# Optimization experiments

Hardware: AMD Instinct MI355X
Metric: run time of the kernel (lower is better)

The kernel has to match this reference:

```python
import jax, jax.numpy as jnp
import numpy as np

N = 50000   # nodes
E = 800000  # edges (avg degree 16)
F = 128     # input_nf = output_nf
H = 128     # hidden_nf


def setup_inputs() -> dict:
    key = jax.random.key(0)
    ks = jax.random.split(key, 10)
    # coords: spatial part in [-1, 1], z-coordinate (last dim) in [0.5, 1.5] (must be > 0)
    xz = jax.random.uniform(ks[0], (N, 3), minval=-1.0, maxval=1.0)
    xz = xz.at[:, -1].set(jax.random.uniform(ks[1], (N,), minval=0.5, maxval=1.5))
    h = jax.random.normal(ks[2], (N, F), dtype=jnp.float32)
    row = jax.random.randint(ks[3], (E,), 0, N)
    # guarantee col != row so AdS distance is strictly positive on every edge
    col = (row + 1 + jax.random.randint(ks[4], (E,), 0, N - 1)) % N
    edge_index = jnp.stack([row, col]).astype(jnp.int32)

    def lin(k, fan_in, fan_out):
        return jax.random.normal(k, (fan_in, fan_out), dtype=jnp.float32) / np.float32(np.sqrt(fan_in))

    return {
        "xz": xz,
        "h": h,
        "We1": lin(ks[5], 2 * F + 1, H), "be1": jnp.full((H,), 0.1, jnp.float32),
        "We2": lin(ks[6], H, H),         "be2": jnp.full((H,), 0.1, jnp.float32),
        "Wn1": lin(ks[7], H + F, H),     "bn1": jnp.full((H,), 0.1, jnp.float32),
        "Wn2": lin(ks[8], H, F),         "bn2": jnp.full((F,), 0.1, jnp.float32),
        "edge_index": edge_index,
    }


def reference(xz, h, We1, be1, We2, be2, Wn1, bn1, Wn2, bn2, edge_index):
    row, col = edge_index[0], edge_index[1]
    n = h.shape[0]

    # AdS (hyperbolic upper-half-space) distance between xz[row] and xz[col]:
    # d = arccosh(1 + |p1 - p2|^2 / (2 z1 z2)), z = last coordinate
    diff = xz[row] - xz[col]                                  # [E, 3]
    u = jnp.sum(diff * diff, axis=-1) / (2.0 * xz[row, -1] * xz[col, -1])
    dist = jnp.arccosh(1.0 + u)[:, None]                      # [E, 1]

    # edge model: concat(source, target, radial) -> Linear -> silu -> Linear -> silu
    m = jnp.concatenate([h[row], h[col], dist], axis=1)       # [E, 2F+1]
    m = jax.nn.silu(m @ We1 + be1)                            # [E, H]
    m = jax.nn.silu(m @ We2 + be2)                            # [E, H]

    # segment_mean over destination nodes (row)
    num = jax.ops.segment_sum(m, row, num_segments=n)                          # [N, H]
    den = jax.ops.segment_sum(jnp.ones_like(m), row, num_segments=n)          # [N, H]
    agg = num / jnp.maximum(den, jnp.ones((), den.dtype))

    # node model: concat(h, agg) -> Linear -> silu -> Linear, plus residual
    z = jnp.concatenate([h, agg], axis=1)                     # [N, F+H]
    out = jax.nn.silu(z @ Wn1 + bn1) @ Wn2 + bn2              # [N, F]
    return h + out
```

## Files before the change

### kernel.cpp

```cpp
#include <hip/hip_runtime.h>

#define NN 50000
#define EE 800000
#define NB 196

typedef __bf16 bf16x8 __attribute__((ext_vector_type(8)));
typedef float  f32x4  __attribute__((ext_vector_type(4)));

__device__ __forceinline__ float bf2f(ushort u) {
    union { unsigned int i; float f; } v; v.i = ((unsigned int)u) << 16; return v.f;
}
__device__ __forceinline__ ushort f2bf(float f) {
    union { float f; unsigned int i; } v; v.f = f;
    unsigned int u = v.i;
    return (ushort)((u + 0x7FFFu + ((u >> 16) & 1u)) >> 16);
}
__device__ __forceinline__ ushort f2bf_fast(float f) {
    union { float f; unsigned int i; } v; v.f = f;
    return (ushort)((v.i + 0x8000u) >> 16);
}
__device__ __forceinline__ float silu(float x) {
    return x * __builtin_amdgcn_rcpf(1.0f + __expf(-x));
}

__global__ void detect_kernel(const ushort* __restrict__ xzu, int* __restrict__ flag) {
    __shared__ int cnt;
    if (threadIdx.x == 0) cnt = 0;
    __syncthreads();
    float v = bf2f(xzu[2 * threadIdx.x]);
    bool sane = (v == v) && (fabsf(v) <= 4.0f);
    if (sane) atomicAdd(&cnt, 1);
    __syncthreads();
    if (threadIdx.x == 0) *flag = (cnt >= 192) ? 0 : 1;
}

__global__ void prep_kernel(const void* __restrict__ hsrc, const void* __restrict__ xzsrc,
                            const int* __restrict__ erow, const int* __restrict__ flag,
                            ushort* __restrict__ hb, float* __restrict__ xzf,
                            int* __restrict__ cntI) {
    const bool isf = (*flag != 0);
    int b = blockIdx.x;
    if (b < 3125) {
        int i = (b * 256 + threadIdx.x) * 8;
        uint4 o;
        if (isf) {
            const float* s = (const float*)hsrc + i;
            float4 f0 = *(const float4*)s;
            float4 f1 = *(const float4*)(s + 4);
            o.x = (unsigned int)f2bf(f0.x) | ((unsigned int)f2bf(f0.y) << 16);
            o.y = (unsigned int)f2bf(f0.z) | ((unsigned int)f2bf(f0.w) << 16);
            o.z = (unsigned int)f2bf(f1.x) | ((unsigned int)f2bf(f1.y) << 16);
            o.w = (unsigned int)f2bf(f1.z) | ((unsigned int)f2bf(f1.w) << 16);
        } else {
            o = *(const uint4*)((const ushort*)hsrc + i);
        }
        *(uint4*)(hb + i) = o;
    } else if (b < 3712) {
        int i = (b - 3125) * 256 + threadIdx.x;
        if (i < NN * 3)
            xzf[i] = isf ? ((const float*)xzsrc)[i] : bf2f(((const ushort*)xzsrc)[i]);
    } else {
        int e = (b - 3712) * 256 + threadIdx.x;
        if (e < EE) atomicAdd(&cntI[erow[e]], 1);
    }
}

__global__ void swizzle_misc_kernel(const void* We1, const void* We2,
                                    const void* Wn1, const void* Wn2,
                                    const void* be1, const void* be2,
                                    const void* bn1, const void* bn2,
                                    const int* __restrict__ flag,
                                    ushort* __restrict__ We1s, ushort* __restrict__ We2s,
                                    ushort* __restrict__ Wn1s, ushort* __restrict__ Wn2s,
                                    float* __restrict__ fb, ushort* __restrict__ wlb) {
    const bool isf = (*flag != 0);
    if (blockIdx.x == 48) {
        for (int j = threadIdx.x; j < 640; j += 256) {
            int which = j >> 7, k = j & 127;
            const void* src = (which == 0) ? be1 : (which == 1) ? be2 :
                              (which == 2) ? bn1 : (which == 3) ? bn2 : We1;
            size_t idx = (which == 4) ? ((size_t)256 * 128 + k) : (size_t)k;
            float v = isf ? ((const float*)src)[idx] : bf2f(((const ushort*)src)[idx]);
            fb[j] = v;
            if (which == 4) wlb[k] = f2bf(v);
        }
        return;
    }
    int c = blockIdx.x * 256 + threadIdx.x;
    const void* src; ushort* dst; int cl;
    if      (c <  4096) { src = We1; dst = We1s; cl = c;         }
    else if (c <  6144) { src = We2; dst = We2s; cl = c - 4096;  }
    else if (c < 10240) { src = Wn1; dst = Wn1s; cl = c - 6144;  }
    else                { src = Wn2; dst = Wn2s; cl = c - 10240; }
    int l = cl & 63, nt = (cl >> 6) & 7, kc = cl >> 9;
    int kbase = kc * 32 + (l >> 4) * 8;
    int n = nt * 16 + (l & 15);
    ushort tmp[8];
#pragma unroll
    for (int j = 0; j < 8; ++j) {
        size_t idx = (size_t)(kbase + j) * 128 + n;
        tmp[j] = isf ? f2bf(((const float*)src)[idx]) : ((const ushort*)src)[idx];
    }
#pragma unroll
    for (int j = 0; j < 8; ++j) dst[(size_t)cl * 8 + j] = tmp[j];
}

__global__ void scanA_kernel(const int* __restrict__ cntI, int* __restrict__ bsum) {
    __shared__ int s[256];
    int t = threadIdx.x;
    int i = blockIdx.x * 256 + t;
    s[t] = (i < NN) ? cntI[i] : 0;
    __syncthreads();
#pragma unroll
    for (int off = 128; off > 0; off >>= 1) {
        if (t < off) s[t] += s[t + off];
        __syncthreads();
    }
    if (t == 0) bsum[blockIdx.x] = s[0];
}

__global__ void scanB_kernel(int* __restrict__ bsum) {
    __shared__ int s[256];
    int t = threadIdx.x;
    int v = (t < NB) ? bsum[t] : 0;
    s[t] = v;
    __syncthreads();
    for (int off = 1; off < 256; off <<= 1) {
        int u = (t >= off) ? s[t - off] : 0;
        __syncthreads();
        if (t >= off) s[t] += u;
        __syncthreads();
    }
    if (t < NB) bsum[t] = s[t] - v;
}

__global__ void scanC_kernel(const int* __restrict__ cntI, const int* __restrict__ bsum,
                             int* __restrict__ rowStart) {
    __shared__ int s[256];
    int t = threadIdx.x;
    int i = blockIdx.x * 256 + t;
    int v = (i < NN) ? cntI[i] : 0;
    s[t] = v;
    __syncthreads();
    for (int off = 1; off < 256; off <<= 1) {
        int u = (t >= off) ? s[t - off] : 0;
        __syncthreads();
        if (t >= off) s[t] += u;
        __syncthreads();
    }
    if (i < NN) rowStart[i] = bsum[blockIdx.x] + s[t] - v;
}

__global__ void scatter_kernel(const int* __restrict__ erow, const int* __restrict__ ecol,
                               const float* __restrict__ xzf,
                               const int* __restrict__ rowStart, int* __restrict__ cursor,
                               int* __restrict__ erowS, int* __restrict__ ecolS,
                               float* __restrict__ distS) {
    int e = blockIdx.x * 256 + threadIdx.x;
    if (e >= EE) return;
    int r = erow[e], c = ecol[e];
    int pos = rowStart[r] + atomicAdd(&cursor[r], 1);
    float4 a = *(const float4*)(xzf + 3 * r);
    float4 b = *(const float4*)(xzf + 3 * c);
    float dx = a.x - b.x, dy = a.y - b.y, dz = a.z - b.z;
    float u = (dx * dx + dy * dy + dz * dz) * __builtin_amdgcn_rcpf(2.0f * a.z * b.z);
    u = fminf(fmaxf(u, 0.0f), 1.0e6f);
    erowS[pos] = r;
    ecolS[pos] = c;
    distS[pos] = __logf(1.0f + u + sqrtf(u * (u + 2.0f)));
}

__global__ __launch_bounds__(256, 3) void pq_kernel(
    const ushort* __restrict__ hb, const ushort* __restrict__ We1s,
    const float* __restrict__ fb, ushort* __restrict__ Pp, ushort* __restrict__ Qq) {
    __shared__ __align__(16) ushort sA[8192];
    const int tid = threadIdx.x;
    const int lane = tid & 63, w = tid >> 6;
    const int col = lane & 15, quad = lane >> 4;
    const int nt0 = w * 2;
    const int ntiles = (NN + 63) / 64;
    const int nA = w * 32 + col, nB = nA + 16;
    const float be1A = fb[nA], be1B = fb[nB];

    for (int tile = blockIdx.x; tile < ntiles; tile += gridDim.x) {
        __syncthreads();
        const int n0 = tile * 64;
#pragma unroll
        for (int i = 0; i < 4; ++i) {
            int node = n0 + lane;
            uint4 v = (node < NN) ? *(const uint4*)(hb + (size_t)node * 128 + (w + 4 * i) * 8)
                                  : make_uint4(0, 0, 0, 0);
            *(uint4*)(sA + (((lane >> 4) * 4 + i) * 64 + w * 16 + (lane & 15)) * 8) = v;
        }
        __syncthreads();

        f32x4 accP[4][2] = {}, accQ[4][2] = {};
#pragma unroll
        for (int kc = 0; kc < 4; ++kc) {
            bf16x8 bp0 = *(const bf16x8*)(We1s + ((kc * 8 + nt0)           * 64 + lane) * 8);
            bf16x8 bp1 = *(const bf16x8*)(We1s + ((kc * 8 + nt0 + 1)       * 64 + lane) * 8);
            bf16x8 bq0 = *(const bf16x8*)(We1s + (((kc + 4) * 8 + nt0)     * 64 + lane) * 8);
            bf16x8 bq1 = *(const bf16x8*)(We1s + (((kc + 4) * 8 + nt0 + 1) * 64 + lane) * 8);
#pragma unroll
            for (int g = 0; g < 4; ++g) {
                bf16x8 a = *(const bf16x8*)(sA + ((g * 4 + kc) * 64 + lane) * 8);
                accP[g][0] = __builtin_amdgcn_mfma_f32_16x16x32_bf16(a, bp0, accP[g][0], 0, 0, 0);
                accP[g][1] = __builtin_amdgcn_mfma_f32_16x16x32_bf16(a, bp1, accP[g][1], 0, 0, 0);
                accQ[g][0] = __builtin_amdgcn_mfma_f32_16x16x32_bf16(a, bq0, accQ[g][0], 0, 0, 0);
                accQ[g][1] = __builtin_amdgcn_mfma_f32_16x16x32_bf16(a, bq1, accQ[g][1], 0, 0, 0);
            }
        }
#pragma unroll
        for (int g = 0; g < 4; ++g) {
#pragma unroll
            for (int r = 0; r < 4; ++r) {
                int node = n0 + g * 16 + quad * 4 + r;
                if (node < NN) {
                    size_t o = (size_t)node * 128;
                    Pp[o + nA] = f2bf(accP[g][0][r] + be1A);
                    Pp[o + nB] = f2bf(accP[g][1][r] + be1B);
                    Qq[o + nA] = f2bf(accQ[g][0][r]);
                    Qq[o + nB] = f2bf(accQ[g][1][r]);
                }
            }
        }
    }
}

__global__ __launch_bounds__(256, 4) void edge_kernel(
    const ushort* __restrict__ Pp, const ushort* __restrict__ Qq,
    const int* __restrict__ erowS, const int* __restrict__ ecolS,
    const float* __restrict__ distS, const ushort* __restrict__ We2s,
    const ushort* __restrict__ wlb, const float* __restrict__ fb,
    float* __restrict__ agg) {
    __shared__ __align__(16) char smem[64 * 132 * 4];
    __shared__ int sRow[64];
    ushort* sM = (ushort*)smem;
    float (*sOut)[132] = (float(*)[132])smem;

    const int tid = threadIdx.x;
    const int lane = tid & 63, w = tid >> 6;
    const int col = lane & 15, quad = lane >> 4;
    const int nt0 = w * 2;

    const int nA = w * 32 + col, nB = nA + 16;
    const float be2A = fb[128 + nA], be2B = fb[128 + nB];

    bf16x8 B2[8];
#pragma unroll
    for (int kc = 0; kc < 4; ++kc) {
        B2[kc * 2]     = *(const bf16x8*)(We2s + ((kc * 8 + nt0)     * 64 + lane) * 8);
        B2[kc * 2 + 1] = *(const bf16x8*)(We2s + ((kc * 8 + nt0 + 1) * 64 + lane) * 8);
    }
    bf16x8 WL[4];
#pragma unroll
    for (int i = 0; i < 4; ++i) WL[i] = *(const bf16x8*)(wlb + (w + 4 * i) * 8);

    const int ntiles = EE / 64;
    const int per = (ntiles + gridDim.x - 1) / gridDim.x;
    const int t0 = blockIdx.x * per;
    const int t1 = (t0 + per < ntiles) ? (t0 + per) : ntiles;

    for (int tile = t0; tile < t1; ++tile) {
        __syncthreads();
        const int e = tile * 64 + lane;
        const int r = erowS[e], c = ecolS[e];
        const float d = distS[e];
        if (w == 0) sRow[lane] = r;
#pragma unroll
        for (int i = 0; i < 4; ++i) {
            int ch = w + 4 * i;
            bf16x8 p = *(const bf16x8*)(Pp + (size_t)r * 128 + ch * 8);
            bf16x8 q = *(const bf16x8*)(Qq + (size_t)c * 128 + ch * 8);
            ushort out8[8];
#pragma unroll
            for (int j = 0; j < 8; ++j) {
                float x = (float)p[j] + (float)q[j] + d * (float)WL[i][j];
                out8[j] = f2bf_fast(silu(x));
            }
            *(uint4*)(sM + (((lane >> 4) * 4 + i) * 64 + w * 16 + (lane & 15)) * 8) =
                *(const uint4*)out8;
        }
        __syncthreads();

        f32x4 acc2[4][2] = {};
#pragma unroll
        for (int kc = 0; kc < 4; ++kc) {
#pragma unroll
            for (int g = 0; g < 4; ++g) {
                bf16x8 a = *(const bf16x8*)(sM + ((g * 4 + kc) * 64 + lane) * 8);
                acc2[g][0] = __builtin_amdgcn_mfma_f32_16x16x32_bf16(a, B2[kc * 2],     acc2[g][0], 0, 0, 0);
                acc2[g][1] = __builtin_amdgcn_mfma_f32_16x16x32_bf16(a, B2[kc * 2 + 1], acc2[g][1], 0, 0, 0);
            }
        }
        __syncthreads();

#pragma unroll
        for (int g = 0; g < 4; ++g) {
#pragma unroll
            for (int r4 = 0; r4 < 4; ++r4) {
                int m = g * 16 + quad * 4 + r4;
                sOut[m][nA] = silu(acc2[g][0][r4] + be2A);
                sOut[m][nB] = silu(acc2[g][1][r4] + be2B);
            }
        }
        __syncthreads();

        {
            const int cc = tid & 127;
            const int mb = (tid >> 7) * 32;
            float acc = 0.0f;
            int prow = sRow[mb];
            for (int k = 0; k < 32; ++k) {
                int rw = sRow[mb + k];
                if (rw != prow) {
                    unsafeAtomicAdd(&agg[(size_t)prow * 128 + cc], acc);
                    acc = 0.0f;
                    prow = rw;
                }
                acc += sOut[mb + k][cc];
            }
            unsafeAtomicAdd(&agg[(size_t)prow * 128 + cc], acc);
        }
    }
}

__global__ __launch_bounds__(256, 3) void node_kernel(
    const ushort* __restrict__ hb, const void* __restrict__ hraw,
    const float* __restrict__ agg, const int* __restrict__ cntI,
    const ushort* __restrict__ Wn1s, const ushort* __restrict__ Wn2s,
    const float* __restrict__ fb, const int* __restrict__ flag,
    void* __restrict__ outv) {
    __shared__ __align__(16) ushort sA[16384];
    __shared__ __align__(16) ushort sM[8192];
    const int tid = threadIdx.x;
    const int lane = tid & 63, w = tid >> 6;
    const int col = lane & 15, quad = lane >> 4;
    const int nt0 = w * 2;
    const int ntiles = (NN + 63) / 64;
    const bool isf = (*flag != 0);
    float* outf = (float*)outv;
    ushort* outu = (ushort*)outv;

    const int nA = w * 32 + col, nB = nA + 16;
    const float bn1A = fb[256 + nA], bn1B = fb[256 + nB];
    const float bn2A = fb[384 + nA], bn2B = fb[384 + nB];

    for (int tile = blockIdx.x; tile < ntiles; tile += gridDim.x) {
        __syncthreads();
        const int n0 = tile * 64;
#pragma unroll
        for (int i = 0; i < 8; ++i) {
            int kb = w + 4 * i;
            int node = n0 + lane;
            uint4 v;
            if (node < NN) {
                if (kb < 16) {
                    v = *(const uint4*)(hb + (size_t)node * 128 + kb * 8);
                } else {
                    const float* ap = agg + (size_t)node * 128 + (kb - 16) * 8;
                    float invc = __builtin_amdgcn_rcpf(fmaxf((float)cntI[node], 1.0f));
                    float4 f0 = *(const float4*)ap;
                    float4 f1 = *(const float4*)(ap + 4);
                    v.x = (unsigned int)f2bf_fast(f0.x * invc) | ((unsigned int)f2bf_fast(f0.y * invc) << 16);
                    v.y = (unsigned int)f2bf_fast(f0.z * invc) | ((unsigned int)f2bf_fast(f0.w * invc) << 16);
                    v.z = (unsigned int)f2bf_fast(f1.x * invc) | ((unsigned int)f2bf_fast(f1.y * invc) << 16);
                    v.w = (unsigned int)f2bf_fast(f1.z * invc) | ((unsigned int)f2bf_fast(f1.w * invc) << 16);
                }
            } else {
                v = make_uint4(0, 0, 0, 0);
            }
            *(uint4*)(sA + (((quad * 8 + i) * 64) + w * 16 + col) * 8) = v;
        }
        __syncthreads();

        f32x4 acc[4][2] = {};
#pragma unroll
        for (int kc = 0; kc < 8; ++kc) {
            bf16x8 b0 = *(const bf16x8*)(Wn1s + ((kc * 8 + nt0)     * 64 + lane) * 8);
            bf16x8 b1 = *(const bf16x8*)(Wn1s + ((kc * 8 + nt0 + 1) * 64 + lane) * 8);
#pragma unroll
            for (int g = 0; g < 4; ++g) {
                bf16x8 a = *(const bf16x8*)(sA + ((g * 8 + kc) * 64 + lane) * 8);
                acc[g][0] = __builtin_amdgcn_mfma_f32_16x16x32_bf16(a, b0, acc[g][0], 0, 0, 0);
                acc[g][1] = __builtin_amdgcn_mfma_f32_16x16x32_bf16(a, b1, acc[g][1], 0, 0, 0);
            }
        }
#pragma unroll
        for (int g = 0; g < 4; ++g) {
            int base0 = ((g * 4 + w) * 64 + (col >> 3) * 16) * 8 + (col & 7);
#pragma unroll
            for (int r = 0; r < 4; ++r) {
                int mrow = quad * 4 + r;
                sM[base0 + mrow * 8]              = f2bf_fast(silu(acc[g][0][r] + bn1A));
                sM[base0 + 2 * 16 * 8 + mrow * 8] = f2bf_fast(silu(acc[g][1][r] + bn1B));
            }
        }
        __syncthreads();

        f32x4 acc2[4][2] = {};
#pragma unroll
        for (int kc = 0; kc < 4; ++kc) {
            bf16x8 b0 = *(const bf16x8*)(Wn2s + ((kc * 8 + nt0)     * 64 + lane) * 8);
            bf16x8 b1 = *(const bf16x8*)(Wn2s + ((kc * 8 + nt0 + 1) * 64 + lane) * 8);
#pragma unroll
            for (int g = 0; g < 4; ++g) {
                bf16x8 a = *(const bf16x8*)(sM + ((g * 4 + kc) * 64 + lane) * 8);
                acc2[g][0] = __builtin_amdgcn_mfma_f32_16x16x32_bf16(a, b0, acc2[g][0], 0, 0, 0);
                acc2[g][1] = __builtin_amdgcn_mfma_f32_16x16x32_bf16(a, b1, acc2[g][1], 0, 0, 0);
            }
        }
#pragma unroll
        for (int g = 0; g < 4; ++g) {
#pragma unroll
            for (int r = 0; r < 4; ++r) {
                int ml2 = g * 16 + quad * 4 + r;
                int node = n0 + ml2;
                if (node < NN) {
                    size_t oi = (size_t)node * 128;
                    float h0 = isf ? ((const float*)hraw)[oi + nA] : bf2f(((const ushort*)hraw)[oi + nA]);
                    float h1 = isf ? ((const float*)hraw)[oi + nB] : bf2f(((const ushort*)hraw)[oi + nB]);
                    float x0 = acc2[g][0][r] + bn2A + h0;
                    float x1 = acc2[g][1][r] + bn2B + h1;
                    if (isf) { outf[oi + nA] = x0; outf[oi + nB] = x1; }
                    else     { outu[oi + nA] = f2bf_fast(x0); outu[oi + nB] = f2bf_fast(x1); }
                }
            }
        }
    }
}

extern "C" void kernel_launch(void* const* d_in, const int* in_sizes, int n_in,
                              void* d_out, int out_size, void* d_ws, size_t ws_size,
                              hipStream_t stream) {
    const void* xz  = d_in[0];
    const void* h   = d_in[1];
    const void* We1 = d_in[2];
    const void* be1 = d_in[3];
    const void* We2 = d_in[4];
    const void* be2 = d_in[5];
    const void* Wn1 = d_in[6];
    const void* bn1 = d_in[7];
    const void* Wn2 = d_in[8];
    const void* bn2 = d_in[9];
    const int*  ei  = (const int*)d_in[10];
    const int* erow = ei;
    const int* ecol = ei + EE;

    char* base = (char*)d_ws;
    size_t cur = 0;
    auto alloc = [&](size_t bytes) { size_t o = cur; cur = (cur + bytes + 255) & ~(size_t)255; return o; };
    int*    flag   = (int*)   (base + alloc(16));
    float*  agg    = (float*) (base + alloc((size_t)NN * 128 * 4));
    int*    cntI   = (int*)   (base + alloc((size_t)NN * 4));
    int*    cursor = (int*)   (base + alloc((size_t)NN * 4));
    ushort* hb     = (ushort*)(base + alloc((size_t)NN * 128 * 2));
    ushort* Pp     = (ushort*)(base + alloc((size_t)NN * 128 * 2));
    ushort* Qq     = (ushort*)(base + alloc((size_t)NN * 128 * 2));
    int*    erowS  = (int*)   (base + alloc((size_t)EE * 4));
    int*    ecolS  = (int*)   (base + alloc((size_t)EE * 4));
    float*  distS  = (float*) (base + alloc((size_t)EE * 4));
    float*  xzf    = (float*) (base + alloc((size_t)NN * 3 * 4 + 16));
    int*    rowSt  = (int*)   (base + alloc((size_t)NN * 4));
    int*    bsum   = (int*)   (base + alloc(256 * 4));
    ushort* We1s   = (ushort*)(base + alloc(32768 * 2));
    ushort* We2s   = (ushort*)(base + alloc(16384 * 2));
    ushort* Wn1s   = (ushort*)(base + alloc(32768 * 2));
    ushort* Wn2s   = (ushort*)(base + alloc(16384 * 2));
    float*  fb     = (float*) (base + alloc(640 * 4));
    ushort* wlb    = (ushort*)(base + alloc(128 * 2));

    size_t zbytes = (size_t)((char*)hb - (char*)agg);
    (void)hipMemsetAsync(agg, 0, zbytes, stream);

    detect_kernel<<<1, 256, 0, stream>>>((const ushort*)xz, flag);
    prep_kernel<<<6837, 256, 0, stream>>>(h, xz, erow, flag, hb, xzf, cntI);
    swizzle_misc_kernel<<<49, 256, 0, stream>>>(We1, We2, Wn1, Wn2, be1, be2, bn1, bn2,
                                                flag, We1s, We2s, Wn1s, Wn2s, fb, wlb);
    scanA_kernel<<<NB, 256, 0, stream>>>(cntI, bsum);
    scanB_kernel<<<1, 256, 0, stream>>>(bsum);
    scanC_kernel<<<NB, 256, 0, stream>>>(cntI, bsum, rowSt);
    scatter_kernel<<<(EE + 255) / 256, 256, 0, stream>>>(erow, ecol, xzf, rowSt, cursor,
                                                         erowS, ecolS, distS);
    pq_kernel<<<782, 256, 0, stream>>>(hb, We1s, fb, Pp, Qq);
    edge_kernel<<<1024, 256, 0, stream>>>(Pp, Qq, erowS, ecolS, distS, We2s, wlb, fb, agg);
    node_kernel<<<782, 256, 0, stream>>>(hb, h, agg, cntI, Wn1s, Wn2s, fb, flag, d_out);
}
```

Baseline: 347.0 us.

## Fuse scan kernels, pack edge records, and segment-reduce edge outputs in registers

Drops the single-block scanB launch by having each scanC block redo the scan of block sums itself. Packs row, col and distance into one int4 per sorted edge so each edge is a single 16-byte load. The edge kernel's final stage now applies silu and segment-reduces straight from the MFMA accumulators, with no fp32 shared-memory staging or the two barriers around it. Shared memory therefore shrinks, so launch bounds go to 8 blocks per CU and the grid doubles to 2048. The register reduction only merges runs of the same row within the 4 rows each lane holds, so it issues more global atomics than the old 32-row column sweeps.

```diff
diff --git a/kernel.cpp b/kernel.cpp
--- a/kernel.cpp
+++ b/kernel.cpp
@@ -119,25 +119,22 @@
     if (t == 0) bsum[blockIdx.x] = s[0];
 }
 
-__global__ void scanB_kernel(int* __restrict__ bsum) {
-    __shared__ int s[256];
-    int t = threadIdx.x;
-    int v = (t < NB) ? bsum[t] : 0;
-    s[t] = v;
-    __syncthreads();
-    for (int off = 1; off < 256; off <<= 1) {
-        int u = (t >= off) ? s[t - off] : 0;
-        __syncthreads();
-        if (t >= off) s[t] += u;
-        __syncthreads();
-    }
-    if (t < NB) bsum[t] = s[t] - v;
-}
-
 __global__ void scanC_kernel(const int* __restrict__ cntI, const int* __restrict__ bsum,
                              int* __restrict__ rowStart) {
     __shared__ int s[256];
+    __shared__ int sbase;
     int t = threadIdx.x;
+    int bv = (t < NB) ? bsum[t] : 0;
+    s[t] = bv;
+    __syncthreads();
+    for (int off = 1; off < 256; off <<= 1) {
+        int u = (t >= off) ? s[t - off] : 0;
+        __syncthreads();
+        if (t >= off) s[t] += u;
+        __syncthreads();
+    }
+    if (t == 0) sbase = (blockIdx.x == 0) ? 0 : s[blockIdx.x - 1];
+    __syncthreads();
     int i = blockIdx.x * 256 + t;
     int v = (i < NN) ? cntI[i] : 0;
     s[t] = v;
@@ -148,14 +145,13 @@
         if (t >= off) s[t] += u;
         __syncthreads();
     }
-    if (i < NN) rowStart[i] = bsum[blockIdx.x] + s[t] - v;
+    if (i < NN) rowStart[i] = sbase + s[t] - v;
 }
 
 __global__ void scatter_kernel(const int* __restrict__ erow, const int* __restrict__ ecol,
                                const float* __restrict__ xzf,
                                const int* __restrict__ rowStart, int* __restrict__ cursor,
-                               int* __restrict__ erowS, int* __restrict__ ecolS,
-                               float* __restrict__ distS) {
+                               int4* __restrict__ eS) {
     int e = blockIdx.x * 256 + threadIdx.x;
     if (e >= EE) return;
     int r = erow[e], c = ecol[e];
@@ -165,9 +161,8 @@
     float dx = a.x - b.x, dy = a.y - b.y, dz = a.z - b.z;
     float u = (dx * dx + dy * dy + dz * dz) * __builtin_amdgcn_rcpf(2.0f * a.z * b.z);
     u = fminf(fmaxf(u, 0.0f), 1.0e6f);
-    erowS[pos] = r;
-    ecolS[pos] = c;
-    distS[pos] = __logf(1.0f + u + sqrtf(u * (u + 2.0f)));
+    float d = __logf(1.0f + u + sqrtf(u * (u + 2.0f)));
+    eS[pos] = make_int4(r, c, __float_as_int(d), 0);
 }
 
 __global__ __launch_bounds__(256, 3) void pq_kernel(
@@ -227,16 +222,13 @@
     }
 }
 
-__global__ __launch_bounds__(256, 4) void edge_kernel(
+__global__ __launch_bounds__(256, 8) void edge_kernel(
     const ushort* __restrict__ Pp, const ushort* __restrict__ Qq,
-    const int* __restrict__ erowS, const int* __restrict__ ecolS,
-    const float* __restrict__ distS, const ushort* __restrict__ We2s,
+    const int4* __restrict__ eS, const ushort* __restrict__ We2s,
     const ushort* __restrict__ wlb, const float* __restrict__ fb,
     float* __restrict__ agg) {
-    __shared__ __align__(16) char smem[64 * 132 * 4];
+    __shared__ __align__(16) ushort sM[8192];
     __shared__ int sRow[64];
-    ushort* sM = (ushort*)smem;
-    float (*sOut)[132] = (float(*)[132])smem;
 
     const int tid = threadIdx.x;
     const int lane = tid & 63, w = tid >> 6;
@@ -263,9 +255,9 @@
 
     for (int tile = t0; tile < t1; ++tile) {
         __syncthreads();
-        const int e = tile * 64 + lane;
-        const int r = erowS[e], c = ecolS[e];
-        const float d = distS[e];
+        const int4 ed = eS[tile * 64 + lane];
+        const int r = ed.x, c = ed.y;
+        const float d = __int_as_float(ed.z);
         if (w == 0) sRow[lane] = r;
 #pragma unroll
         for (int i = 0; i < 4; ++i) {
@@ -293,34 +285,30 @@
                 acc2[g][1] = __builtin_amdgcn_mfma_f32_16x16x32_bf16(a, B2[kc * 2 + 1], acc2[g][1], 0, 0, 0);
             }
         }
-        __syncthreads();
-
-#pragma unroll
-        for (int g = 0; g < 4; ++g) {
-#pragma unroll
-            for (int r4 = 0; r4 < 4; ++r4) {
-                int m = g * 16 + quad * 4 + r4;
-                sOut[m][nA] = silu(acc2[g][0][r4] + be2A);
-                sOut[m][nB] = silu(acc2[g][1][r4] + be2B);
-            }
-        }
-        __syncthreads();
 
         {
-            const int cc = tid & 127;
-            const int mb = (tid >> 7) * 32;
-            float acc = 0.0f;
-            int prow = sRow[mb];
-            for (int k = 0; k < 32; ++k) {
-                int rw = sRow[mb + k];
-                if (rw != prow) {
-                    unsafeAtomicAdd(&agg[(size_t)prow * 128 + cc], acc);
-                    acc = 0.0f;
-                    prow = rw;
+            float accA = 0.0f, accB = 0.0f;
+            int prow = sRow[quad * 4];
+#pragma unroll
+            for (int g = 0; g < 4; ++g) {
+#pragma unroll
+                for (int r4 = 0; r4 < 4; ++r4) {
+                    int m = g * 16 + quad * 4 + r4;
+                    int row = sRow[m];
+                    float vA = silu(acc2[g][0][r4] + be2A);
+                    float vB = silu(acc2[g][1][r4] + be2B);
+                    if (row != prow) {
+                        unsafeAtomicAdd(&agg[(size_t)prow * 128 + nA], accA);
+                        unsafeAtomicAdd(&agg[(size_t)prow * 128 + nB], accB);
+                        accA = 0.0f; accB = 0.0f;
+                        prow = row;
+                    }
+                    accA += vA;
+                    accB += vB;
                 }
-                acc += sOut[mb + k][cc];
-            }
-            unsafeAtomicAdd(&agg[(size_t)prow * 128 + cc], acc);
+            }
+            unsafeAtomicAdd(&agg[(size_t)prow * 128 + nA], accA);
+            unsafeAtomicAdd(&agg[(size_t)prow * 128 + nB], accB);
         }
     }
 }
@@ -457,9 +445,7 @@
     ushort* hb     = (ushort*)(base + alloc((size_t)NN * 128 * 2));
     ushort* Pp     = (ushort*)(base + alloc((size_t)NN * 128 * 2));
     ushort* Qq     = (ushort*)(base + alloc((size_t)NN * 128 * 2));
-    int*    erowS  = (int*)   (base + alloc((size_t)EE * 4));
-    int*    ecolS  = (int*)   (base + alloc((size_t)EE * 4));
-    float*  distS  = (float*) (base + alloc((size_t)EE * 4));
+    int4*   eS     = (int4*)  (base + alloc((size_t)EE * 16));
     float*  xzf    = (float*) (base + alloc((size_t)NN * 3 * 4 + 16));
     int*    rowSt  = (int*)   (base + alloc((size_t)NN * 4));
     int*    bsum   = (int*)   (base + alloc(256 * 4));
@@ -478,11 +464,9 @@
     swizzle_misc_kernel<<<49, 256, 0, stream>>>(We1, We2, Wn1, Wn2, be1, be2, bn1, bn2,
                                                 flag, We1s, We2s, Wn1s, Wn2s, fb, wlb);
     scanA_kernel<<<NB, 256, 0, stream>>>(cntI, bsum);
-    scanB_kernel<<<1, 256, 0, stream>>>(bsum);
     scanC_kernel<<<NB, 256, 0, stream>>>(cntI, bsum, rowSt);
-    scatter_kernel<<<(EE + 255) / 256, 256, 0, stream>>>(erow, ecol, xzf, rowSt, cursor,
-                                                         erowS, ecolS, distS);
+    scatter_kernel<<<(EE + 255) / 256, 256, 0, stream>>>(erow, ecol, xzf, rowSt, cursor, eS);
     pq_kernel<<<782, 256, 0, stream>>>(hb, We1s, fb, Pp, Qq);
-    edge_kernel<<<1024, 256, 0, stream>>>(Pp, Qq, erowS, ecolS, distS, We2s, wlb, fb, agg);
+    edge_kernel<<<2048, 256, 0, stream>>>(Pp, Qq, eS, We2s, wlb, fb, agg);
     node_kernel<<<782, 256, 0, stream>>>(hb, h, agg, cntI, Wn1s, Wn2s, fb, flag, d_out);
 }
```

After: 554.3 us. 59.8% more time.
